# Performance work log

Measured on AMD Instinct MI355X. Metric: run time of the kernel, lower is better.

## Reference

```python
import jax, jax.numpy as jnp
import numpy as np

N, D_IN, D_EMB, K = 16384, 1024, 256, 1024
ALPHA, EPS = 0.01, 1e-5


def setup_inputs() -> dict:
    key = jax.random.key(0)
    ks = jax.random.split(key, 6)
    inp = jax.random.normal(ks[0], (N, D_IN), dtype=jnp.float32)
    W_send = jax.random.normal(ks[1], (D_IN, D_EMB), dtype=jnp.float32) / np.sqrt(D_IN)
    b_send = jnp.zeros((D_EMB,), dtype=jnp.float32)
    W_recv = jax.random.normal(ks[2], (D_EMB, D_IN), dtype=jnp.float32) / np.sqrt(D_EMB)
    b_recv = jnp.zeros((D_IN,), dtype=jnp.float32)
    codebook = jax.random.normal(ks[3], (K, D_EMB), dtype=jnp.float32)
    ema_vecs = codebook.copy()
    ema_size = jnp.zeros((K,), dtype=jnp.float32)
    return {"input": inp, "W_send": W_send, "b_send": b_send,
            "W_recv": W_recv, "b_recv": b_recv, "codebook": codebook,
            "ema_vecs": ema_vecs, "ema_size": ema_size}


def reference(input, W_send, b_send, W_recv, b_recv, codebook, ema_vecs, ema_size):
    sg = jax.lax.stop_gradient
    # send projection -> latent z  [N, D_EMB]
    z = input @ W_send + b_send
    # nearest-neighbor lookup: argmin_k ||e_k||^2 - 2 <z, e_k>
    sqr = jnp.sum(codebook * codebook, axis=1)          # [K]
    cov = jnp.einsum('nj,kj->nk', z, codebook)          # [N, K]
    codes = jnp.argmin(sqr - 2.0 * cov, axis=-1)        # [N] int
    # fetch embeddings (gather)
    vectors = codebook[codes]                            # [N, D_EMB]
    # mse losses, reduction='sum'
    embedding = jnp.sum((vectors - sg(z)) ** 2)
    commitment = jnp.sum((z - sg(vectors)) ** 2)
    # straight-through output
    emb_out = z + sg(vectors - z)
    # EMA accumulate (one-hot scatter == segment_sum)
    upd_vecs = jax.ops.segment_sum(z, codes, num_segments=K)              # [K, D_EMB]
    upd_size = jax.ops.segment_sum(jnp.ones((z.shape[0],), z.dtype), codes, num_segments=K)
    ema_vecs_new = ema_vecs + ALPHA * (upd_vecs - ema_vecs)
    ema_size_new = ema_size + ALPHA * (upd_size - ema_size)
    # EMA update (Laplace-smoothed centroid)
    n = jnp.sum(ema_size_new)
    coef = n / (n + K * EPS)
    size = coef * (ema_size_new + EPS)
    weight_new = ema_vecs_new / size[:, None]
    # empirical entropy of the codes in bits
    prob = jnp.bincount(codes, length=K).astype(jnp.float32) / codes.size
    ent = -jnp.sum(jnp.where(prob > 0, prob * jnp.log(prob), 0.0)) / jnp.log(2.0)
    # recv projection
    x = emb_out @ W_recv + b_recv
    return (x, codes, embedding, commitment, ent, ema_vecs_new, ema_size_new, weight_new)
```

## Files before the change

kernel.cpp:

```cpp
#include <hip/hip_runtime.h>
#include <math.h>

#define NROWS 16384
#define DIN   1024
#define DEMB  256
#define KC    1024
#define ALPHA 0.01f
#define EPSV  1e-5f
#define INV2048 4.8828125e-4f
#define CHUNK 32
#define COV_CHUNKS 8

typedef _Float16 f16;
typedef __attribute__((ext_vector_type(4)))  _Float16 f16x4;
typedef __attribute__((ext_vector_type(8)))  _Float16 f16x8;
typedef __attribute__((ext_vector_type(16))) float    f32x16;
typedef unsigned long long u64;

#define OFF_Z       0
#define OFF_R       4194304
#define OFF_SQR     5242880
#define OFF_ZH      5243904
#define OFF_ZL      7341056
#define OFF_WTH     9438208
#define OFF_WTL     9569280
#define OFF_CBH     9700352
#define OFF_CBL     9831424
#define OFF_KEYS    9962496
#define OFF_CODES   9995264
#define OFF_LIST    10011648
#define OFF_OFFS    10028032
#define OFF_UPD     10029056
#define OFF_HIST    10291200
#define OFF_CURSOR  10292224
#define OFF_LOSS    10293248
#define OFF_COUNTSF 10293264
#define OFF_SIZE    10294288

#define OUT_X      0
#define OUT_CODES  16777216
#define OUT_EMB    16793600
#define OUT_COMMIT 16793601
#define OUT_ENT    16793602
#define OUT_EMAV   16793603
#define OUT_EMAS   17055747
#define OUT_W      17056771

__device__ __forceinline__ void split_f32(float x, f16& h, f16& l) {
    h = (f16)x;
    l = (f16)((x - (float)h) * 2048.0f);
}

__global__ __launch_bounds__(256) void prep_kernel(const float* __restrict__ W_send,
                                                   const float* __restrict__ W_recv,
                                                   const float* __restrict__ cb,
                                                   float* __restrict__ ws) {
    const int b = blockIdx.x;
    const int t = threadIdx.x;
    int* wsi = (int*)ws;

    if (b < 256) {
        f16* wth = (f16*)(ws + OFF_WTH);
        f16* wtl = (f16*)(ws + OFF_WTL);
        const int n = b;
        f16x4 h4, l4;
#pragma unroll
        for (int j = 0; j < 4; ++j) {
            int k = t * 4 + j;
            float x = W_send[(size_t)k * DEMB + n];
            f16 h, l; split_f32(x, h, l);
            h4[j] = h; l4[j] = l;
        }
        *(f16x4*)&wth[(size_t)n * DIN + t * 4] = h4;
        *(f16x4*)&wtl[(size_t)n * DIN + t * 4] = l4;
    } else if (b < 512) {
        f16* cbh = (f16*)(ws + OFF_CBH);
        f16* cbl = (f16*)(ws + OFF_CBL);
        int idx = ((b - 256) * 256 + t) * 4;
        float4 v = *(const float4*)&cb[idx];
        f16x4 h4, l4;
        f16 h, l;
        split_f32(v.x, h, l); h4[0] = h; l4[0] = l;
        split_f32(v.y, h, l); h4[1] = h; l4[1] = l;
        split_f32(v.z, h, l); h4[2] = h; l4[2] = l;
        split_f32(v.w, h, l); h4[3] = h; l4[3] = l;
        *(f16x4*)&cbh[idx] = h4;
        *(f16x4*)&cbl[idx] = l4;
    } else if (b < 768) {
        f16* wrh = (f16*)(ws + OFF_ZH);
        f16* wrl = (f16*)(ws + OFF_ZH + 131072);
        const int n = (b - 512) * 4 + (t >> 6);
        const int lane = t & 63;
        f16x4 h4, l4;
#pragma unroll
        for (int j = 0; j < 4; ++j) {
            int k = lane * 4 + j;
            float x = W_recv[(size_t)k * DIN + n];
            f16 h, l; split_f32(x, h, l);
            h4[j] = h; l4[j] = l;
        }
        *(f16x4*)&wrh[(size_t)n * DEMB + lane * 4] = h4;
        *(f16x4*)&wrl[(size_t)n * DEMB + lane * 4] = l4;
    } else if (b < 1024) {
        float* sqr = ws + OFF_SQR;
        const int k = (b - 768) * 4 + (t >> 6);
        const int lane = t & 63;
        float4 v = ((const float4*)cb)[k * 64 + lane];
        float s = v.x * v.x + v.y * v.y + v.z * v.z + v.w * v.w;
        for (int off = 32; off > 0; off >>= 1) s += __shfl_down(s, off, 64);
        if (lane == 0) sqr[k] = s;
    } else if (b < 1280) {
        float4 zed = make_float4(0.f, 0.f, 0.f, 0.f);
        *(float4*)&ws[OFF_UPD + (size_t)(b - 1024) * 1024 + t * 4] = zed;
    } else if (b == 1280) {
#pragma unroll
        for (int j = 0; j < 4; ++j) {
            wsi[OFF_HIST + t * 4 + j] = 0;
            wsi[OFF_CURSOR + t * 4 + j] = 0;
        }
        if (t < 16) ws[OFF_LOSS + t] = 0.f;
    } else {
        u64* keys = (u64*)(ws + OFF_KEYS);
        keys[(b - 1281) * 256 + t] = ~0ull;
    }
}

__global__ __launch_bounds__(512) void gemm1_mfma(const float* __restrict__ in,
                                                  const f16* __restrict__ wth,
                                                  const f16* __restrict__ wtl,
                                                  const float* __restrict__ bsend,
                                                  float* __restrict__ z,
                                                  f16* __restrict__ zh,
                                                  f16* __restrict__ zl) {
    __shared__ f16 sm[2 * 2 * 2 * 128 * 64];
    const int tid = threadIdx.x;
    const int wave = tid >> 6, lane = tid & 63;
    const int half = lane >> 5, l31 = lane & 31;
    const int wrow = wave >> 2, wcol = wave & 3;

    const int L = blockIdx.x;
    const int v = L >> 3;
    const int bx = v & 1;
    const int by = (L & 7) + 8 * (v >> 1);
    const int rowBase = by * 128;
    const int colBase = bx * 128;

    const int sr  = tid >> 2;
    const int skq = tid & 3;
    const int sr7 = sr & 7;

    f32x16 accm[2] = {};
    f32x16 accx[2] = {};

    auto stageB = [&](int buf, int ks) {
#pragma unroll
        for (int i = 0; i < 4; ++i) {
            const int q  = wave * 4 + i;
            const int hl = q >> 4;
            const int c  = (q & 15) * 8 + (lane >> 3);
            const int p  = lane & 7;
            const int s  = p ^ (c & 7);
            const f16* src = (hl ? wtl : wth)
                           + (size_t)(colBase + c) * DIN + ks + s * 8;
            f16* dst = sm + buf * 32768 + 16384 + q * 512 + lane * 8;
            __builtin_amdgcn_global_load_lds(
                (const __attribute__((address_space(1))) void*)src,
                (__attribute__((address_space(3))) void*)dst, 16, 0, 0);
        }
    };

    auto loadA = [&](int ks, float4* av) {
        const float* src = &in[(size_t)(rowBase + sr) * DIN + ks + skq * 16];
#pragma unroll
        for (int j = 0; j < 4; ++j) av[j] = ((const float4*)src)[j];
    };

    auto writeA = [&](int buf, const float4* av) {
        f16* Abase = sm + buf * 32768;
#pragma unroll
        for (int q = 0; q < 2; ++q) {
            f16x8 h8, l8;
#pragma unroll
            for (int j = 0; j < 2; ++j) {
                float4 v4 = av[q * 2 + j];
                f16 h, l;
                split_f32(v4.x, h, l); h8[j * 4 + 0] = h; l8[j * 4 + 0] = l;
                split_f32(v4.y, h, l); h8[j * 4 + 1] = h; l8[j * 4 + 1] = l;
                split_f32(v4.z, h, l); h8[j * 4 + 2] = h; l8[j * 4 + 2] = l;
                split_f32(v4.w, h, l); h8[j * 4 + 3] = h; l8[j * 4 + 3] = l;
            }
            const int s = skq * 2 + q;
            const int off = sr * 64 + ((s ^ sr7) << 3);
            *(f16x8*)&Abase[off] = h8;
            *(f16x8*)&Abase[8192 + off] = l8;
        }
    };

    auto compute = [&](int buf) {
        const f16* Ah = sm + buf * 32768;
        const f16* Al = Ah + 8192;
        const f16* Bh = Ah + 16384;
        const f16* Bl = Ah + 24576;
        const int c  = wcol * 32 + l31;
        const int c7 = c & 7;
#pragma unroll
        for (int t4 = 0; t4 < 4; ++t4) {
            const int s = t4 * 2 + half;
            f16x8 a_h[2], a_l[2];
#pragma unroll
            for (int rt = 0; rt < 2; ++rt) {
                const int r = wrow * 64 + rt * 32 + l31;
                const int off = r * 64 + ((s ^ (r & 7)) << 3);
                a_h[rt] = *(const f16x8*)&Ah[off];
                a_l[rt] = *(const f16x8*)&Al[off];
            }
            const int boff = c * 64 + ((s ^ c7) << 3);
            f16x8 b_h = *(const f16x8*)&Bh[boff];
            f16x8 b_l = *(const f16x8*)&Bl[boff];
#pragma unroll
            for (int rt = 0; rt < 2; ++rt) {
                accm[rt] = __builtin_amdgcn_mfma_f32_32x32x16_f16(a_h[rt], b_h, accm[rt], 0, 0, 0);
                accx[rt] = __builtin_amdgcn_mfma_f32_32x32x16_f16(a_h[rt], b_l, accx[rt], 0, 0, 0);
                accx[rt] = __builtin_amdgcn_mfma_f32_32x32x16_f16(a_l[rt], b_h, accx[rt], 0, 0, 0);
            }
        }
    };

    stageB(0, 0);
    {
        float4 av[4];
        loadA(0, av);
        writeA(0, av);
    }
    __syncthreads();

    int cur = 0;
    for (int step = 0; step < 16; ++step) {
        float4 av[4];
        const bool pf = (step + 1) < 16;
        if (pf) {
            stageB(cur ^ 1, (step + 1) * 64);
            loadA((step + 1) * 64, av);
        }
        compute(cur);
        if (pf) writeA(cur ^ 1, av);
        __syncthreads();
        cur ^= 1;
    }

#pragma unroll
    for (int rt = 0; rt < 2; ++rt) {
        const int col = colBase + wcol * 32 + l31;
        const float bb = bsend[col];
#pragma unroll
        for (int reg = 0; reg < 16; ++reg) {
            const int row = rowBase + wrow * 64 + rt * 32 + (reg & 3) + 8 * (reg >> 2) + 4 * half;
            const float zv = accm[rt][reg] + INV2048 * accx[rt][reg] + bb;
            const size_t o = (size_t)row * DEMB + col;
            z[o] = zv;
            f16 h = (f16)zv;
            zh[o] = h;
            zl[o] = (f16)((zv - (float)h) * 2048.0f);
        }
    }
}

__global__ __launch_bounds__(256, 2) void gemm2_mfma(const f16* __restrict__ cbh,
                                                     const f16* __restrict__ cbl,
                                                     const f16* __restrict__ wrh,
                                                     const f16* __restrict__ wrl,
                                                     float* __restrict__ R) {
    __shared__ f16 sm[16384];
    const int tid = threadIdx.x;
    const int wave = tid >> 6, lane = tid & 63;
    const int half = lane >> 5, l31 = lane & 31;
    const int wr = wave >> 1, wc = wave & 1;
    const int rowBase = blockIdx.y * 64;
    const int colBase = blockIdx.x * 64;

    f32x16 accm = {}, accx = {};

    for (int step = 0; step < 4; ++step) {
        const int ks = step * 64;
        __syncthreads();
#pragma unroll
        for (int i = 0; i < 8; ++i) {
            const int q   = wave * 8 + i;
            const int arr = q >> 3;
            const int grp = q & 7;
            const int r   = grp * 8 + (lane >> 3);
            const int p   = lane & 7;
            const int s   = p ^ (r & 7);
            const f16* basep = (arr == 0) ? cbh : (arr == 1) ? cbl
                             : (arr == 2) ? wrh : wrl;
            const int rowg = ((arr >= 2) ? colBase : rowBase) + r;
            const f16* src = basep + (size_t)rowg * DEMB + ks + s * 8;
            f16* dst = sm + arr * 4096 + grp * 512;
            __builtin_amdgcn_global_load_lds(
                (const __attribute__((address_space(1))) void*)src,
                (__attribute__((address_space(3))) void*)dst, 16, 0, 0);
        }
        __syncthreads();
#pragma unroll
        for (int t = 0; t < 4; ++t) {
            const int sgi = t * 2 + half;
            const int ar = wr * 32 + l31;
            const int bc = wc * 32 + l31;
            const int aoff = ar * 64 + ((sgi ^ (ar & 7)) << 3);
            const int boff = bc * 64 + ((sgi ^ (bc & 7)) << 3);
            f16x8 a_h = *(const f16x8*)&sm[aoff];
            f16x8 a_l = *(const f16x8*)&sm[4096 + aoff];
            f16x8 b_h = *(const f16x8*)&sm[8192 + boff];
            f16x8 b_l = *(const f16x8*)&sm[12288 + boff];
            accm = __builtin_amdgcn_mfma_f32_32x32x16_f16(a_h, b_h, accm, 0, 0, 0);
            accx = __builtin_amdgcn_mfma_f32_32x32x16_f16(a_h, b_l, accx, 0, 0, 0);
            accx = __builtin_amdgcn_mfma_f32_32x32x16_f16(a_l, b_h, accx, 0, 0, 0);
        }
    }

    const int col = colBase + wc * 32 + l31;
#pragma unroll
    for (int reg = 0; reg < 16; ++reg) {
        const int row = rowBase + wr * 32 + (reg & 3) + 8 * (reg >> 2) + 4 * half;
        R[(size_t)row * DIN + col] = accm[reg] + INV2048 * accx[reg];
    }
}

__device__ __forceinline__ void cov_stage(const f16* __restrict__ cbh,
                                          const f16* __restrict__ cbl,
                                          f16* sC, int buf, int codeBase,
                                          int wave, int lane) {
#pragma unroll
    for (int i = 0; i < 8; ++i) {
        const int seg = wave * 8 + i;
        const int hl  = seg >> 4;
        const int rp  = seg & 15;
        const int r   = rp * 2 + (lane >> 5);
        const f16* src = (hl ? cbl : cbh)
                       + (size_t)(codeBase + r) * DEMB
                       + (((lane & 31) ^ r) << 3);
        f16* dst = sC + (((buf << 1) + hl) * 32 + rp * 2) * DEMB;
        __builtin_amdgcn_global_load_lds(
            (const __attribute__((address_space(1))) void*)src,
            (__attribute__((address_space(3))) void*)dst,
            16, 0, 0);
    }
}

__global__ __launch_bounds__(256, 2) void cov_mfma_kernel(const f16* __restrict__ zh,
                                                          const f16* __restrict__ zl,
                                                          const f16* __restrict__ cbh,
                                                          const f16* __restrict__ cbl,
                                                          const float* __restrict__ sqr,
                                                          u64* __restrict__ keys) {
    __shared__ f16 sC[2 * 2 * 32 * DEMB];
    const int tid = threadIdx.x;
    const int wave = tid >> 6, lane = tid & 63;
    const int half = lane >> 5, l31 = lane & 31;

    const int L = blockIdx.x;
    const int v = L >> 3;
    const int bx = v & 3;
    const int by = (L & 7) + 8 * (v >> 2);

    const int rowBase = by * 128 + wave * 32;
    const int myRow = rowBase + l31;
    const int cb0 = bx * (COV_CHUNKS * 32);

    cov_stage(cbh, cbl, sC, 0, cb0, wave, lane);

    f16x8 a_h[16], a_l[16];
#pragma unroll
    for (int t = 0; t < 16; ++t) {
        size_t o = (size_t)myRow * DEMB + t * 16 + half * 8;
        a_h[t] = *(const f16x8*)&zh[o];
        a_l[t] = *(const f16x8*)&zl[o];
    }

    float runv[16];
    int   runc[16];
#pragma unroll
    for (int r = 0; r < 16; ++r) { runv[r] = 3.4e38f; runc[r] = 0; }

    for (int cc = 0; cc < COV_CHUNKS; ++cc) {
        __syncthreads();
        if (cc + 1 < COV_CHUNKS)
            cov_stage(cbh, cbl, sC, (cc + 1) & 1, cb0 + (cc + 1) * 32, wave, lane);

        const f16* Ch = sC + ((cc & 1) * 2 + 0) * 32 * DEMB;
        const f16* Cl = sC + ((cc & 1) * 2 + 1) * 32 * DEMB;

        f32x16 accm = {};
        f32x16 accx = {};
#pragma unroll
        for (int t = 0; t < 16; ++t) {
            const int seg = t * 2 + half;
            const int p = ((seg ^ l31) << 3);
            f16x8 b_h = *(const f16x8*)&Ch[l31 * DEMB + p];
            f16x8 b_l = *(const f16x8*)&Cl[l31 * DEMB + p];
            accm = __builtin_amdgcn_mfma_f32_32x32x16_f16(a_h[t], b_h, accm, 0, 0, 0);
            accx = __builtin_amdgcn_mfma_f32_32x32x16_f16(a_h[t], b_l, accx, 0, 0, 0);
            accx = __builtin_amdgcn_mfma_f32_32x32x16_f16(a_l[t], b_h, accx, 0, 0, 0);
        }

        const int code = cb0 + cc * 32 + l31;
        const float sqv = sqr[code];
#pragma unroll
        for (int r = 0; r < 16; ++r) {
            float s = sqv - 2.0f * (accm[r] + INV2048 * accx[r]);
            if (s < runv[r]) { runv[r] = s; runc[r] = code; }
        }
    }

#pragma unroll
    for (int r = 0; r < 16; ++r) {
        float v2 = runv[r]; int ci = runc[r];
        for (int off = 16; off > 0; off >>= 1) {
            float ov = __shfl_down(v2, off, 32);
            int   oc = __shfl_down(ci, off, 32);
            if (ov < v2 || (ov == v2 && oc < ci)) { v2 = ov; ci = oc; }
        }
        if (l31 == 0) {
            int row = rowBase + (r & 3) + 8 * (r >> 2) + 4 * half;
            unsigned ub = __float_as_uint(v2);
            ub = (ub & 0x80000000u) ? ~ub : (ub | 0x80000000u);
            u64 key = ((u64)ub << 32) | (unsigned)ci;
            atomicMin(&keys[row], key);
        }
    }
}

__global__ __launch_bounds__(256) void decode_kernel(const u64* __restrict__ keys,
                                                     int* __restrict__ codes,
                                                     float* __restrict__ out_codes,
                                                     int* __restrict__ hist) {
    int r = blockIdx.x * 256 + threadIdx.x;
    int c = (int)(keys[r] & 0xFFFFFFFFull);
    codes[r] = c;
    out_codes[r] = (float)c;
    atomicAdd(&hist[c], 1);
}

__global__ __launch_bounds__(1024) void prefix_kernel(const int* __restrict__ hist,
                                                      int* __restrict__ offs,
                                                      float* __restrict__ countsf) {
    __shared__ int s[1024];
    int t = threadIdx.x;
    int v = hist[t];
    s[t] = v;
    countsf[t] = (float)v;
    __syncthreads();
    for (int d = 1; d < 1024; d <<= 1) {
        int x = (t >= d) ? s[t - d] : 0;
        __syncthreads();
        s[t] += x;
        __syncthreads();
    }
    offs[t] = s[t] - v;
}

__global__ __launch_bounds__(256) void fill_kernel(const int* __restrict__ codes,
                                                   const int* __restrict__ offs,
                                                   int* __restrict__ cursor,
                                                   int* __restrict__ list) {
    int r = blockIdx.x * 256 + threadIdx.x;
    int c = codes[r];
    int pos = offs[c] + atomicAdd(&cursor[c], 1);
    list[pos] = r;
}

__global__ __launch_bounds__(256) void upd_loss_kernel(const float* __restrict__ z,
                                                       const float* __restrict__ cb,
                                                       const int* __restrict__ list,
                                                       const int* __restrict__ codes,
                                                       float* __restrict__ upd,
                                                       float* __restrict__ loss) {
    __shared__ int srow[CHUNK];
    __shared__ int scode[CHUNK];
    const int tid = threadIdx.x;
    const int base = blockIdx.x * CHUNK;
    if (tid < CHUNK) {
        int r = list[base + tid];
        srow[tid] = r;
        scode[tid] = codes[r];
    }
    __syncthreads();

    int cur = scode[0];
    float cbv = cb[(size_t)cur * DEMB + tid];
    float acc = 0.f, lacc = 0.f;
    float zv = z[(size_t)srow[0] * DEMB + tid];
#pragma unroll 4
    for (int i = 0; i < CHUNK; ++i) {
        float znext = (i + 1 < CHUNK) ? z[(size_t)srow[i + 1] * DEMB + tid] : 0.f;
        int c = scode[i];
        if (c != cur) {
            atomicAdd(&upd[(size_t)cur * DEMB + tid], acc);
            acc = 0.f;
            cur = c;
            cbv = cb[(size_t)cur * DEMB + tid];
        }
        acc += zv;
        float d = zv - cbv;
        lacc += d * d;
        zv = znext;
    }
    atomicAdd(&upd[(size_t)cur * DEMB + tid], acc);

    __shared__ float red[256];
    red[tid] = lacc;
    __syncthreads();
    for (int s = 128; s > 0; s >>= 1) {
        if (tid < s) red[tid] += red[tid + s];
        __syncthreads();
    }
    if (tid == 0) atomicAdd(loss, red[0]);
}

__global__ __launch_bounds__(256) void recv_kernel(const float* __restrict__ R,
                                                   const float* __restrict__ brecv,
                                                   const int* __restrict__ codes,
                                                   float* __restrict__ out) {
    const int n = blockIdx.x;
    const int t = threadIdx.x;
    const int code = codes[n];
    float4 r = ((const float4*)(R + (size_t)code * DIN))[t];
    float4 b = ((const float4*)brecv)[t];
    ((float4*)(out + (size_t)n * DIN))[t] =
        make_float4(r.x + b.x, r.y + b.y, r.z + b.z, r.w + b.w);
}

__global__ __launch_bounds__(1024) void ema_small_kernel(const float* __restrict__ ema_size,
                                                         const float* __restrict__ counts,
                                                         const float* __restrict__ loss,
                                                         float* __restrict__ size_ws,
                                                         float* __restrict__ out) {
    __shared__ float rn[1024];
    __shared__ float re[1024];
    const int k = threadIdx.x;
    float c  = counts[k];
    float es = ema_size[k];
    float esn = es + ALPHA * (c - es);
    out[OUT_EMAS + k] = esn;
    float p = c * (1.0f / (float)NROWS);
    rn[k] = esn;
    re[k] = (p > 0.f) ? p * logf(p) : 0.f;
    __syncthreads();
    for (int s = 512; s > 0; s >>= 1) {
        if (k < s) { rn[k] += rn[k + s]; re[k] += re[k + s]; }
        __syncthreads();
    }
    float n = rn[0];
    float coef = n / (n + (float)KC * EPSV);
    size_ws[k] = coef * (esn + EPSV);
    if (k == 0) {
        out[OUT_ENT] = -re[0] / logf(2.0f);
        float l = loss[0];
        out[OUT_EMB] = l;
        out[OUT_COMMIT] = l;
    }
}

__global__ __launch_bounds__(256) void emav_kernel(const float* __restrict__ ema_vecs,
                                                   const float* __restrict__ upd,
                                                   const float* __restrict__ size_ws,
                                                   float* __restrict__ out) {
    int idx = blockIdx.x * 256 + threadIdx.x;
    float ev = ema_vecs[idx], uv = upd[idx];
    float evn = ev + ALPHA * (uv - ev);
    out[OUT_EMAV + idx] = evn;
    out[OUT_W + idx] = evn / size_ws[idx >> 8];
}

extern "C" void kernel_launch(void* const* d_in, const int* in_sizes, int n_in,
                              void* d_out, int out_size, void* d_ws, size_t ws_size,
                              hipStream_t stream) {
    const float* input    = (const float*)d_in[0];
    const float* W_send   = (const float*)d_in[1];
    const float* b_send   = (const float*)d_in[2];
    const float* W_recv   = (const float*)d_in[3];
    const float* b_recv   = (const float*)d_in[4];
    const float* codebook = (const float*)d_in[5];
    const float* ema_vecs = (const float*)d_in[6];
    const float* ema_size = (const float*)d_in[7];
    float* out = (float*)d_out;
    float* ws  = (float*)d_ws;
    int*   wsi = (int*)d_ws;

    f16* wth = (f16*)(ws + OFF_WTH);
    f16* wtl = (f16*)(ws + OFF_WTL);
    f16* cbh = (f16*)(ws + OFF_CBH);
    f16* cbl = (f16*)(ws + OFF_CBL);
    f16* zh  = (f16*)(ws + OFF_ZH);
    f16* zl  = (f16*)(ws + OFF_ZL);
    u64* keys = (u64*)(ws + OFF_KEYS);
    f16* wrh = (f16*)(ws + OFF_ZH);
    f16* wrl = (f16*)(ws + OFF_ZH + 131072);

    prep_kernel<<<1345, 256, 0, stream>>>(W_send, W_recv, codebook, ws);

    gemm2_mfma<<<dim3(DIN / 64, KC / 64), 256, 0, stream>>>(
        cbh, cbl, wrh, wrl, ws + OFF_R);

    gemm1_mfma<<<(DEMB / 128) * (NROWS / 128), 512, 0, stream>>>(
        input, wth, wtl, b_send, ws + OFF_Z, zh, zl);

    cov_mfma_kernel<<<(KC / (COV_CHUNKS * 32)) * (NROWS / 128), 256, 0, stream>>>(
        zh, zl, cbh, cbl, ws + OFF_SQR, keys);

    decode_kernel<<<NROWS / 256, 256, 0, stream>>>(
        keys, wsi + OFF_CODES, out + OUT_CODES, wsi + OFF_HIST);

    prefix_kernel<<<1, 1024, 0, stream>>>(
        wsi + OFF_HIST, wsi + OFF_OFFS, ws + OFF_COUNTSF);

    fill_kernel<<<NROWS / 256, 256, 0, stream>>>(
        wsi + OFF_CODES, wsi + OFF_OFFS, wsi + OFF_CURSOR, wsi + OFF_LIST);

    upd_loss_kernel<<<NROWS / CHUNK, 256, 0, stream>>>(
        ws + OFF_Z, codebook, wsi + OFF_LIST, wsi + OFF_CODES,
        ws + OFF_UPD, ws + OFF_LOSS);

    recv_kernel<<<NROWS, 256, 0, stream>>>(
        ws + OFF_R, b_recv, wsi + OFF_CODES, out + OUT_X);

    ema_small_kernel<<<1, 1024, 0, stream>>>(
        ema_size, ws + OFF_COUNTSF, ws + OFF_LOSS, ws + OFF_SIZE, out);

    emav_kernel<<<KC, 256, 0, stream>>>(
        ema_vecs, ws + OFF_UPD, ws + OFF_SIZE, out);
}
```

Baseline: 253.0 us.

## Shrink gemm1 tile to 64 rows, single-buffer LDS for higher occupancy

Reworks the input-projection GEMM to use 64x128 tiles with 256 threads and a single LDS buffer instead of 128x128 tiles with 512 threads and double buffering. It launches twice as many blocks and targets three blocks per CU, relying on more resident waves to hide global-load latency in place of explicit software prefetch. In exchange, B tiles are reloaded twice as often across blocks, and each step now waits on loads with no overlap inside a block.

```diff
diff --git a/kernel.cpp b/kernel.cpp
--- a/kernel.cpp
+++ b/kernel.cpp
@@ -125,24 +125,24 @@
     }
 }
 
-__global__ __launch_bounds__(512) void gemm1_mfma(const float* __restrict__ in,
-                                                  const f16* __restrict__ wth,
-                                                  const f16* __restrict__ wtl,
-                                                  const float* __restrict__ bsend,
-                                                  float* __restrict__ z,
-                                                  f16* __restrict__ zh,
-                                                  f16* __restrict__ zl) {
-    __shared__ f16 sm[2 * 2 * 2 * 128 * 64];
+__global__ __launch_bounds__(256, 3) void gemm1_mfma(const float* __restrict__ in,
+                                                     const f16* __restrict__ wth,
+                                                     const f16* __restrict__ wtl,
+                                                     const float* __restrict__ bsend,
+                                                     float* __restrict__ z,
+                                                     f16* __restrict__ zh,
+                                                     f16* __restrict__ zl) {
+    __shared__ f16 sm[24576];
     const int tid = threadIdx.x;
     const int wave = tid >> 6, lane = tid & 63;
     const int half = lane >> 5, l31 = lane & 31;
-    const int wrow = wave >> 2, wcol = wave & 3;
+    const int wr = wave >> 1, wc = wave & 1;
 
     const int L = blockIdx.x;
     const int v = L >> 3;
     const int bx = v & 1;
     const int by = (L & 7) + 8 * (v >> 1);
-    const int rowBase = by * 128;
+    const int rowBase = by * 64;
     const int colBase = bx * 128;
 
     const int sr  = tid >> 2;
@@ -152,110 +152,93 @@
     f32x16 accm[2] = {};
     f32x16 accx[2] = {};
 
-    auto stageB = [&](int buf, int ks) {
-#pragma unroll
-        for (int i = 0; i < 4; ++i) {
-            const int q  = wave * 4 + i;
+    for (int step = 0; step < 16; ++step) {
+        const int ks = step * 64;
+
+#pragma unroll
+        for (int i = 0; i < 8; ++i) {
+            const int q  = wave * 8 + i;
             const int hl = q >> 4;
-            const int c  = (q & 15) * 8 + (lane >> 3);
+            const int c0 = (q & 15) * 8;
+            const int col = c0 + (lane >> 3);
             const int p  = lane & 7;
-            const int s  = p ^ (c & 7);
+            const int s  = p ^ (col & 7);
             const f16* src = (hl ? wtl : wth)
-                           + (size_t)(colBase + c) * DIN + ks + s * 8;
-            f16* dst = sm + buf * 32768 + 16384 + q * 512 + lane * 8;
+                           + (size_t)(colBase + col) * DIN + ks + s * 8;
+            f16* dst = sm + 8192 + hl * 8192 + c0 * 64;
             __builtin_amdgcn_global_load_lds(
                 (const __attribute__((address_space(1))) void*)src,
                 (__attribute__((address_space(3))) void*)dst, 16, 0, 0);
         }
-    };
-
-    auto loadA = [&](int ks, float4* av) {
-        const float* src = &in[(size_t)(rowBase + sr) * DIN + ks + skq * 16];
-#pragma unroll
-        for (int j = 0; j < 4; ++j) av[j] = ((const float4*)src)[j];
-    };
-
-    auto writeA = [&](int buf, const float4* av) {
-        f16* Abase = sm + buf * 32768;
-#pragma unroll
-        for (int q = 0; q < 2; ++q) {
+
+        {
+            const float* srcp = &in[(size_t)(rowBase + sr) * DIN + ks + skq * 16];
+            float4 av0 = ((const float4*)srcp)[0];
+            float4 av1 = ((const float4*)srcp)[1];
+            float4 av2 = ((const float4*)srcp)[2];
+            float4 av3 = ((const float4*)srcp)[3];
+            f16 h, l;
             f16x8 h8, l8;
-#pragma unroll
-            for (int j = 0; j < 2; ++j) {
-                float4 v4 = av[q * 2 + j];
-                f16 h, l;
-                split_f32(v4.x, h, l); h8[j * 4 + 0] = h; l8[j * 4 + 0] = l;
-                split_f32(v4.y, h, l); h8[j * 4 + 1] = h; l8[j * 4 + 1] = l;
-                split_f32(v4.z, h, l); h8[j * 4 + 2] = h; l8[j * 4 + 2] = l;
-                split_f32(v4.w, h, l); h8[j * 4 + 3] = h; l8[j * 4 + 3] = l;
+            split_f32(av0.x, h, l); h8[0] = h; l8[0] = l;
+            split_f32(av0.y, h, l); h8[1] = h; l8[1] = l;
+            split_f32(av0.z, h, l); h8[2] = h; l8[2] = l;
+            split_f32(av0.w, h, l); h8[3] = h; l8[3] = l;
+            split_f32(av1.x, h, l); h8[4] = h; l8[4] = l;
+            split_f32(av1.y, h, l); h8[5] = h; l8[5] = l;
+            split_f32(av1.z, h, l); h8[6] = h; l8[6] = l;
+            split_f32(av1.w, h, l); h8[7] = h; l8[7] = l;
+            const int o0 = sr * 64 + (((2 * skq + 0) ^ sr7) << 3);
+            *(f16x8*)&sm[o0] = h8;
+            *(f16x8*)&sm[4096 + o0] = l8;
+
+            split_f32(av2.x, h, l); h8[0] = h; l8[0] = l;
+            split_f32(av2.y, h, l); h8[1] = h; l8[1] = l;
+            split_f32(av2.z, h, l); h8[2] = h; l8[2] = l;
+            split_f32(av2.w, h, l); h8[3] = h; l8[3] = l;
+            split_f32(av3.x, h, l); h8[4] = h; l8[4] = l;
+            split_f32(av3.y, h, l); h8[5] = h; l8[5] = l;
+            split_f32(av3.z, h, l); h8[6] = h; l8[6] = l;
+            split_f32(av3.w, h, l); h8[7] = h; l8[7] = l;
+            const int o1 = sr * 64 + (((2 * skq + 1) ^ sr7) << 3);
+            *(f16x8*)&sm[o1] = h8;
+            *(f16x8*)&sm[4096 + o1] = l8;
+        }
+
+        __syncthreads();
+
+        {
+            const int r = wr * 32 + l31;
+            const int r7 = r & 7;
+#pragma unroll
+            for (int t4 = 0; t4 < 4; ++t4) {
+                const int s = t4 * 2 + half;
+                const int aoff = r * 64 + ((s ^ r7) << 3);
+                f16x8 a_h = *(const f16x8*)&sm[aoff];
+                f16x8 a_l = *(const f16x8*)&sm[4096 + aoff];
+#pragma unroll
+                for (int ct = 0; ct < 2; ++ct) {
+                    const int c = wc * 64 + ct * 32 + l31;
+                    const int boff = c * 64 + ((s ^ (c & 7)) << 3);
+                    f16x8 b_h = *(const f16x8*)&sm[8192 + boff];
+                    f16x8 b_l = *(const f16x8*)&sm[16384 + boff];
+                    accm[ct] = __builtin_amdgcn_mfma_f32_32x32x16_f16(a_h, b_h, accm[ct], 0, 0, 0);
+                    accx[ct] = __builtin_amdgcn_mfma_f32_32x32x16_f16(a_h, b_l, accx[ct], 0, 0, 0);
+                    accx[ct] = __builtin_amdgcn_mfma_f32_32x32x16_f16(a_l, b_h, accx[ct], 0, 0, 0);
+                }
             }
-            const int s = skq * 2 + q;
-            const int off = sr * 64 + ((s ^ sr7) << 3);
-            *(f16x8*)&Abase[off] = h8;
-            *(f16x8*)&Abase[8192 + off] = l8;
-        }
-    };
-
-    auto compute = [&](int buf) {
-        const f16* Ah = sm + buf * 32768;
-        const f16* Al = Ah + 8192;
-        const f16* Bh = Ah + 16384;
-        const f16* Bl = Ah + 24576;
-        const int c  = wcol * 32 + l31;
-        const int c7 = c & 7;
-#pragma unroll
-        for (int t4 = 0; t4 < 4; ++t4) {
-            const int s = t4 * 2 + half;
-            f16x8 a_h[2], a_l[2];
-#pragma unroll
-            for (int rt = 0; rt < 2; ++rt) {
-                const int r = wrow * 64 + rt * 32 + l31;
-                const int off = r * 64 + ((s ^ (r & 7)) << 3);
-                a_h[rt] = *(const f16x8*)&Ah[off];
-                a_l[rt] = *(const f16x8*)&Al[off];
-            }
-            const int boff = c * 64 + ((s ^ c7) << 3);
-            f16x8 b_h = *(const f16x8*)&Bh[boff];
-            f16x8 b_l = *(const f16x8*)&Bl[boff];
-#pragma unroll
-            for (int rt = 0; rt < 2; ++rt) {
-                accm[rt] = __builtin_amdgcn_mfma_f32_32x32x16_f16(a_h[rt], b_h, accm[rt], 0, 0, 0);
-                accx[rt] = __builtin_amdgcn_mfma_f32_32x32x16_f16(a_h[rt], b_l, accx[rt], 0, 0, 0);
-                accx[rt] = __builtin_amdgcn_mfma_f32_32x32x16_f16(a_l[rt], b_h, accx[rt], 0, 0, 0);
-            }
-        }
-    };
-
-    stageB(0, 0);
-    {
-        float4 av[4];
-        loadA(0, av);
-        writeA(0, av);
-    }
-    __syncthreads();
-
-    int cur = 0;
-    for (int step = 0; step < 16; ++step) {
-        float4 av[4];
-        const bool pf = (step + 1) < 16;
-        if (pf) {
-            stageB(cur ^ 1, (step + 1) * 64);
-            loadA((step + 1) * 64, av);
-        }
-        compute(cur);
-        if (pf) writeA(cur ^ 1, av);
-        __syncthreads();
-        cur ^= 1;
-    }
-
-#pragma unroll
-    for (int rt = 0; rt < 2; ++rt) {
-        const int col = colBase + wcol * 32 + l31;
+        }
+
+        __syncthreads();
+    }
+
+#pragma unroll
+    for (int ct = 0; ct < 2; ++ct) {
+        const int col = colBase + wc * 64 + ct * 32 + l31;
         const float bb = bsend[col];
 #pragma unroll
         for (int reg = 0; reg < 16; ++reg) {
-            const int row = rowBase + wrow * 64 + rt * 32 + (reg & 3) + 8 * (reg >> 2) + 4 * half;
-            const float zv = accm[rt][reg] + INV2048 * accx[rt][reg] + bb;
+            const int row = rowBase + wr * 32 + (reg & 3) + 8 * (reg >> 2) + 4 * half;
+            const float zv = accm[ct][reg] + INV2048 * accx[ct][reg] + bb;
             const size_t o = (size_t)row * DEMB + col;
             z[o] = zv;
             f16 h = (f16)zv;
@@ -602,7 +585,7 @@
     gemm2_mfma<<<dim3(DIN / 64, KC / 64), 256, 0, stream>>>(
         cbh, cbl, wrh, wrl, ws + OFF_R);
 
-    gemm1_mfma<<<(DEMB / 128) * (NROWS / 128), 512, 0, stream>>>(
+    gemm1_mfma<<<(DEMB / 128) * (NROWS / 64), 256, 0, stream>>>(
         input, wth, wtl, b_send, ws + OFF_Z, zh, zl);
 
     cov_mfma_kernel<<<(KC / (COV_CHUNKS * 32)) * (NROWS / 128), 256, 0, stream>>>(
```

Result: slower. 258.3 us (+2.1%).
